# Kernel optimization log

Measured on AMD Instinct MI355X. Metric: run time of the kernel, lower is better.

Reference implementation:

```python
import jax, jax.numpy as jnp
import numpy as np
from jax import lax

B, T, N, H, NC = 2, 8, 512, 64, 10
NEG = -1e9
LN_EPS = 1e-5


def _gatv2(x, mask, Wl, Wr, att, b):
    # GATv2Conv (PyG semantics, eval mode): e_ij = att . leaky_relu(Wr x_i + Wl x_j),
    # softmax over source nodes j with self-loops, out_i = sum_j alpha_ij * (Wl x_j).
    # x: (B, N, Fin); mask: (N, N) bool adjacency incl. self-loops; att: (heads, C).
    heads, C = att.shape
    Bn, Nn, _ = x.shape
    xl = (x @ Wl).reshape(Bn, Nn, heads, C)  # source transform
    xr = (x @ Wr).reshape(Bn, Nn, heads, C)  # target transform
    s = jax.nn.leaky_relu(xr[:, :, None] + xl[:, None, :], 0.2)  # (B, Ni, Nj, h, C)
    e = jnp.einsum('bijhc,hc->bijh', s, att)
    e = jnp.where(mask[None, :, :, None], e, NEG)
    alpha = jax.nn.softmax(e, axis=2)  # softmax over neighbors j
    out = jnp.einsum('bijh,bjhc->bihc', alpha, xl)
    return out.reshape(Bn, Nn, heads * C) + b


def _gru_layer(x, Wih, Whh, bih, bhh):
    # torch nn.GRU single layer, batch_first; x: (B, T, Hin)
    h0 = jnp.zeros((x.shape[0], Whh.shape[0]), x.dtype)
    def step(h, xt):
        gi = xt @ Wih + bih
        gh = h @ Whh + bhh
        ir, iz, inn = jnp.split(gi, 3, axis=-1)
        hr, hz, hn = jnp.split(gh, 3, axis=-1)
        r = jax.nn.sigmoid(ir + hr)
        z = jax.nn.sigmoid(iz + hz)
        n = jnp.tanh(inn + r * hn)
        hnew = (1.0 - z) * n + z * h
        return hnew, hnew
    _, ys = lax.scan(step, h0, jnp.swapaxes(x, 0, 1))
    return jnp.swapaxes(ys, 0, 1)


def setup_inputs() -> dict:
    key = jax.random.key(0)
    ks = jax.random.split(key, 20)
    def rn(i, shape, s=0.1):
        return jax.random.normal(ks[i], shape, jnp.float32) * s
    x_seq = jax.random.normal(ks[0], (B, T, N, 1), jnp.float32)
    a = jax.random.uniform(ks[1], (N, N))
    up = jnp.triu((a > 0.95).astype(jnp.float32), 1)
    static_adj = up + up.T  # sparse symmetric 0/1 static graph
    dyn_W = jax.random.normal(ks[2], (N, N), jnp.float32)
    reg_lambda = jnp.array([0.05], jnp.float32)
    return {
        'x_seq': x_seq, 'static_adj': static_adj, 'dyn_W': dyn_W, 'reg_lambda': reg_lambda,
        'g1_Wl': rn(3, (1, H)), 'g1_Wr': rn(4, (1, H)), 'g1_att': rn(5, (4, H // 4)), 'g1_b': jnp.zeros(H),
        'g2_Wl': rn(6, (H, H)), 'g2_Wr': rn(7, (H, H)), 'g2_att': rn(8, (1, H)), 'g2_b': jnp.zeros(H),
        'gru_Wih0': rn(9, (H, 3 * H)), 'gru_Whh0': rn(10, (H, 3 * H)), 'gru_bih0': jnp.zeros(3 * H), 'gru_bhh0': jnp.zeros(3 * H),
        'gru_Wih1': rn(11, (H, 3 * H)), 'gru_Whh1': rn(12, (H, 3 * H)), 'gru_bih1': jnp.zeros(3 * H), 'gru_bhh1': jnp.zeros(3 * H),
        'attn_W': rn(13, (H, 1)), 'attn_b': jnp.zeros(1),
        'cls_W1': rn(14, (H, H)), 'cls_b1': jnp.zeros(H), 'ln_g': jnp.ones(H), 'ln_b': jnp.zeros(H),
        'cls_W2': rn(15, (H, NC)), 'cls_b2': jnp.zeros(NC),
    }


def reference(x_seq, static_adj, dyn_W, reg_lambda,
              g1_Wl, g1_Wr, g1_att, g1_b, g2_Wl, g2_Wr, g2_att, g2_b,
              gru_Wih0, gru_Whh0, gru_bih0, gru_bhh0,
              gru_Wih1, gru_Whh1, gru_bih1, gru_bhh1,
              attn_W, attn_b, cls_W1, cls_b1, ln_g, ln_b, cls_W2, cls_b2):
    Bn, Tn, Nn, _ = x_seq.shape
    lam = jnp.maximum(reg_lambda[0], 0.01)
    t = jnp.arange(Tn, dtype=x_seq.dtype)
    gts = jnp.exp(-lam * t)  # gating values per timestep
    dyn = jax.nn.relu(dyn_W + dyn_W.T)
    fused = gts[:, None, None] * static_adj + (1.0 - gts)[:, None, None] * dyn  # (T, N, N)
    masks = (fused > 0) | jnp.eye(Nn, dtype=bool)[None]  # edge set + self-loops

    def step(carry, inp):
        xt, mask = inp  # xt: (B, N, 1)
        h = jax.nn.elu(_gatv2(xt, mask, g1_Wl, g1_Wr, g1_att, g1_b))
        h = jax.nn.elu(_gatv2(h, mask, g2_Wl, g2_Wr, g2_att, g2_b))
        return carry, h.mean(axis=1)  # (B, H) graph readout

    _, reps = lax.scan(step, 0.0, (jnp.swapaxes(x_seq, 0, 1), masks))
    h_seq = jnp.swapaxes(reps, 0, 1)  # (B, T, H)

    gru_out = _gru_layer(h_seq, gru_Wih0, gru_Whh0, gru_bih0, gru_bhh0)
    gru_out = _gru_layer(gru_out, gru_Wih1, gru_Whh1, gru_bih1, gru_bhh1)

    att_scores = jax.nn.softmax((gru_out @ attn_W + attn_b)[..., 0], axis=1)  # (B, T)
    final = jnp.einsum('bt,bth->bh', att_scores, gru_out)

    z = final @ cls_W1 + cls_b1
    mu = jnp.mean(z, axis=-1, keepdims=True)
    var = jnp.var(z, axis=-1, keepdims=True)
    z = (z - mu) / jnp.sqrt(var + LN_EPS) * ln_g + ln_b
    z = jax.nn.gelu(z, approximate=False)
    logits = z @ cls_W2 + cls_b2
    return logits, gts, att_scores
```

## Files before the change

kernel.cpp:

```cpp
#include <hip/hip_runtime.h>
#include <math.h>

#define BB 2
#define TT 8
#define NN 512
#define HH 64
#define NC 10

typedef unsigned char uchar;

__device__ __forceinline__ float elu1(float v){ return v > 0.f ? v : expm1f(v); }
__device__ __forceinline__ float sigm(float v){ return 1.f/(1.f+expf(-v)); }

__global__ __launch_bounds__(256) void k_mask(
    const float* __restrict__ dW, const float* __restrict__ sadj,
    uchar* __restrict__ M0, uchar* __restrict__ M1,
    float* __restrict__ Z2, float* __restrict__ hseq,
    const float* __restrict__ att1, const float* __restrict__ Wr1,
    const float* __restrict__ Wl1, float* __restrict__ AB,
    const float* __restrict__ Whh0, const float* __restrict__ Wih1,
    const float* __restrict__ Whh1, float4* __restrict__ WT4)
{
    __shared__ float tr[64][65];
    int bx = blockIdx.x, by = blockIdx.y;
    int tid = threadIdx.x;
    if (blockIdx.z == 1){
        int idx = (by*8 + bx)*256 + tid;
        if (idx < 3*4096){
            int m = idx >> 12, r = idx & 4095;
            int gg = r >> 6, k = r & 63;
            const float* W = (m == 0) ? Whh0 : (m == 1) ? Wih1 : Whh1;
            float4 o;
            o.x = W[k*192 + gg];
            o.y = W[k*192 + 64 + gg];
            o.z = W[k*192 + 128 + gg];
            o.w = 0.f;
            WT4[(size_t)m*4096 + r] = o;
        }
        return;
    }
    int i0 = by*64, j0 = bx*64;
    #pragma unroll
    for (int q = 0; q < 4; ++q){
        int r = (tid >> 4) + 16*q, c4 = tid & 15;
        float4 v = *(const float4*)&dW[(size_t)(j0+r)*NN + i0 + 4*c4];
        tr[r][4*c4+0] = v.x; tr[r][4*c4+1] = v.y;
        tr[r][4*c4+2] = v.z; tr[r][4*c4+3] = v.w;
    }
    __syncthreads();
    #pragma unroll
    for (int q = 0; q < 4; ++q){
        int row = (tid >> 4) + 16*q, c4 = tid & 15;
        int i = i0 + row, j = j0 + 4*c4;
        float4 d  = *(const float4*)&dW[(size_t)i*NN + j];
        float4 sa = *(const float4*)&sadj[(size_t)i*NN + j];
        uchar4 m0, m1;
        float dd0 = d.x + tr[4*c4+0][row];
        float dd1 = d.y + tr[4*c4+1][row];
        float dd2 = d.z + tr[4*c4+2][row];
        float dd3 = d.w + tr[4*c4+3][row];
        m0.x = (sa.x > 0.f) || (i == j+0);
        m0.y = (sa.y > 0.f) || (i == j+1);
        m0.z = (sa.z > 0.f) || (i == j+2);
        m0.w = (sa.w > 0.f) || (i == j+3);
        m1.x = m0.x || (dd0 > 0.f);
        m1.y = m0.y || (dd1 > 0.f);
        m1.z = m0.z || (dd2 > 0.f);
        m1.w = m0.w || (dd3 > 0.f);
        *(uchar4*)&M0[(size_t)i*NN + j] = m0;
        *(uchar4*)&M1[(size_t)i*NN + j] = m1;
    }
    int flat = (by*8 + bx)*256 + tid;
    if (flat < BB*TT*NN) Z2[flat] = 0.f;
    else if (flat < BB*TT*NN + BB*TT*HH) hseq[flat - BB*TT*NN] = 0.f;
    if (bx == 0 && by == 0 && tid < 8){
        int h = tid & 3;
        const float* W = (tid < 4) ? Wr1 : Wl1;
        float s = 0.f;
        for (int c = 0; c < 16; ++c) s += att1[h*16+c]*W[h*16+c];
        AB[tid] = s;
    }
}

__global__ __launch_bounds__(256) void k_gat1f(
    const float* __restrict__ x_seq, const uchar* __restrict__ M0,
    const uchar* __restrict__ M1,
    const float* __restrict__ Wl, const float* __restrict__ Wr,
    const float* __restrict__ att, const float* __restrict__ bias,
    const float* __restrict__ AB,
    const float* __restrict__ Wl2, const float* __restrict__ Wr2,
    const float* __restrict__ att2,
    float* __restrict__ xl2, float* __restrict__ xr2,
    float* __restrict__ ui, float* __restrict__ vj)
{
    __shared__ float x_s[NN];
    __shared__ float S_s[4][4];
    __shared__ float h_s[4][HH];
    __shared__ float Wl2_s[64*64];
    __shared__ float Wr2_s[64*64];
    int bt = blockIdx.y; int t = bt % TT;
    int i0 = blockIdx.x * 4;
    int tid = threadIdx.x;
    int il = tid >> 6, jl = tid & 63;
    int i = i0 + il;
    const uchar* M = t ? M1 : M0;
    ((float2*)x_s)[tid] = ((const float2*)(x_seq + bt*NN))[tid];
    #pragma unroll
    for (int q = 0; q < 4; ++q){
        int idx = q*256 + tid;
        ((float4*)Wl2_s)[idx] = ((const float4*)Wl2)[idx];
        ((float4*)Wr2_s)[idx] = ((const float4*)Wr2)[idx];
    }
    __syncthreads();
    float xi = x_s[i];
    const uchar* Mrow = M + (size_t)i*NN;
    float xj[8], msk[8];
    #pragma unroll
    for (int jj = 0; jj < 8; ++jj){
        int j = jj*64 + jl;
        xj[jj] = x_s[j];
        msk[jj] = Mrow[j] ? 1.f : 0.f;
    }
    float sw[4] = {0,0,0,0}, swx[4] = {0,0,0,0};
    for (int h = 0; h < 4; ++h){
        float acc[8] = {0,0,0,0,0,0,0,0};
        #pragma unroll
        for (int c = 0; c < 16; ++c){
            int hc = h*16 + c;
            float wl = Wl[hc];
            float q  = 0.4f * att[hc];
            float pr = xi * Wr[hc];
            #pragma unroll
            for (int jj = 0; jj < 8; ++jj){
                float s = fmaf(xj[jj], wl, pr);
                acc[jj] = fmaf(q, fabsf(s), acc[jj]);
            }
        }
        float lin = 0.6f * xi * AB[h];
        float al6 = 0.6f * AB[4+h];
        #pragma unroll
        for (int jj = 0; jj < 8; ++jj){
            float e = acc[jj] + fmaf(al6, xj[jj], lin);
            float w = msk[jj] * __expf(e);
            sw[h] += w;
            swx[h] = fmaf(w, xj[jj], swx[h]);
        }
    }
    #pragma unroll
    for (int off = 32; off; off >>= 1){
        #pragma unroll
        for (int h = 0; h < 4; ++h){
            sw[h]  += __shfl_down(sw[h],  off);
            swx[h] += __shfl_down(swx[h], off);
        }
    }
    if (jl == 0){
        #pragma unroll
        for (int h = 0; h < 4; ++h) S_s[il][h] = swx[h] / sw[h];
    }
    __syncthreads();
    {
        int hc = tid & 63, row = tid >> 6;
        float v = S_s[row][hc >> 4] * Wl[hc] + bias[hc];
        h_s[row][hc] = elu1(v);
    }
    __syncthreads();
    {
        int c = tid & 63, row = tid >> 6;
        float al = 0.f, ar = 0.f;
        #pragma unroll 8
        for (int k = 0; k < 64; ++k){
            float hv = h_s[row][k];
            al = fmaf(hv, Wl2_s[k*64 + c], al);
            ar = fmaf(hv, Wr2_s[k*64 + c], ar);
        }
        size_t ridx = (size_t)(bt*NN + i0 + row);
        xl2[ridx*HH + c] = al;
        xr2[ridx*HH + c] = ar;
        float a2 = att2[c];
        float pu = a2 * ar, pv = a2 * al;
        #pragma unroll
        for (int off = 32; off; off >>= 1){
            pu += __shfl_down(pu, off);
            pv += __shfl_down(pv, off);
        }
        if (c == 0){ ui[ridx] = pu; vj[ridx] = pv; }
    }
}

__global__ __launch_bounds__(256) void k_e2(
    const float* __restrict__ xl2, const float* __restrict__ xr2,
    const uchar* __restrict__ M0, const uchar* __restrict__ M1,
    const float* __restrict__ att,
    const float* __restrict__ ui, const float* __restrict__ vj,
    float* __restrict__ WgT, float* __restrict__ Z2)
{
    __shared__ float xrT[64][68];
    __shared__ float xlT[64][68];
    int bt = blockIdx.z, t = bt % TT;
    int i0 = blockIdx.y*64, j0 = blockIdx.x*64;
    int base = bt*NN;
    int tid = threadIdx.x;
    const uchar* M = t ? M1 : M0;
    {
        int r = tid >> 2;
        #pragma unroll
        for (int q = 0; q < 4; ++q){
            int c4 = (tid & 3) + 4*q;
            float4 a = *(const float4*)&xr2[(size_t)(base+i0+r)*HH + 4*c4];
            float4 b = *(const float4*)&xl2[(size_t)(base+j0+r)*HH + 4*c4];
            xrT[4*c4+0][r] = a.x; xrT[4*c4+1][r] = a.y;
            xrT[4*c4+2][r] = a.z; xrT[4*c4+3][r] = a.w;
            xlT[4*c4+0][r] = b.x; xlT[4*c4+1][r] = b.y;
            xlT[4*c4+2][r] = b.z; xlT[4*c4+3][r] = b.w;
        }
    }
    int ti = tid >> 4, tj = tid & 15;
    int iL = ti*4, jL = tj*4;
    float4 u4 = *(const float4*)&ui[base+i0+iL];
    float4 v4 = *(const float4*)&vj[base+j0+jL];
    float uu[4] = {u4.x, u4.y, u4.z, u4.w};
    float vv[4] = {v4.x, v4.y, v4.z, v4.w};
    float acc[4][4];
    #pragma unroll
    for (int ii = 0; ii < 4; ++ii)
        #pragma unroll
        for (int jj = 0; jj < 4; ++jj)
            acc[ii][jj] = 0.6f*(uu[ii] + vv[jj]);
    __syncthreads();
    #pragma unroll 8
    for (int c = 0; c < 64; ++c){
        float qa = 0.4f * att[c];
        float4 a4 = *(const float4*)&xrT[c][iL];
        float4 b4 = *(const float4*)&xlT[c][jL];
        float a[4] = {a4.x, a4.y, a4.z, a4.w};
        float b[4] = {b4.x, b4.y, b4.z, b4.w};
        #pragma unroll
        for (int ii = 0; ii < 4; ++ii)
            #pragma unroll
            for (int jj = 0; jj < 4; ++jj)
                acc[ii][jj] = fmaf(qa, fabsf(a[ii] + b[jj]), acc[ii][jj]);
    }
    float w[4][4];
    #pragma unroll
    for (int ii = 0; ii < 4; ++ii){
        int i = i0 + iL + ii;
        uchar4 mr = *(const uchar4*)&M[(size_t)i*NN + j0 + jL];
        w[ii][0] = mr.x ? __expf(acc[ii][0]) : 0.f;
        w[ii][1] = mr.y ? __expf(acc[ii][1]) : 0.f;
        w[ii][2] = mr.z ? __expf(acc[ii][2]) : 0.f;
        w[ii][3] = mr.w ? __expf(acc[ii][3]) : 0.f;
    }
    #pragma unroll
    for (int jj = 0; jj < 4; ++jj){
        int j = j0 + jL + jj;
        float4 wv = { w[0][jj], w[1][jj], w[2][jj], w[3][jj] };
        *(float4*)&WgT[(size_t)(base+j)*NN + i0 + iL] = wv;
    }
    #pragma unroll
    for (int ii = 0; ii < 4; ++ii){
        float zi = w[ii][0] + w[ii][1] + w[ii][2] + w[ii][3];
        zi += __shfl_down(zi, 8);
        zi += __shfl_down(zi, 4);
        zi += __shfl_down(zi, 2);
        zi += __shfl_down(zi, 1);
        if (tj == 0) atomicAdd(&Z2[base + i0 + iL + ii], zi);
    }
}

__global__ __launch_bounds__(256) void k_a2(
    const float* __restrict__ WgT, const float* __restrict__ xl2,
    const float* __restrict__ Z2, const float* __restrict__ bias,
    float* __restrict__ hseq)
{
    __shared__ float a_s[64][20];
    __shared__ float x_s[64][68];
    __shared__ float msum[64];
    int bt = blockIdx.y;
    int i0 = blockIdx.x * 16;
    int base = bt * NN;
    int tid = threadIdx.x;
    int tg = tid >> 4, tc = tid & 15;
    if (tid < 64) msum[tid] = 0.f;
    float4 acc = {0,0,0,0};
    for (int jc = 0; jc < 8; ++jc){
        int j0 = jc*64;
        {
            int row = tid >> 2, c4 = tid & 3;
            ((float4*)&a_s[row][0])[c4] = ((const float4*)&WgT[(size_t)(base+j0+row)*NN + i0])[c4];
        }
        #pragma unroll
        for (int q = 0; q < 4; ++q){
            int idx = q*256 + tid; int row = idx >> 4, c4 = idx & 15;
            ((float4*)&x_s[row][0])[c4] = ((const float4*)&xl2[(size_t)(base+j0+row)*HH])[c4];
        }
        __syncthreads();
        #pragma unroll 8
        for (int j = 0; j < 64; ++j){
            float a = a_s[j][tg];
            float4 xv = ((float4*)&x_s[j][0])[tc];
            acc.x = fmaf(a, xv.x, acc.x);
            acc.y = fmaf(a, xv.y, acc.y);
            acc.z = fmaf(a, xv.z, acc.z);
            acc.w = fmaf(a, xv.w, acc.w);
        }
        __syncthreads();
    }
    float rz = 1.f / Z2[base + i0 + tg];
    float4 b4 = ((const float4*)bias)[tc];
    float4 h;
    h.x = elu1(acc.x*rz + b4.x);
    h.y = elu1(acc.y*rz + b4.y);
    h.z = elu1(acc.z*rz + b4.z);
    h.w = elu1(acc.w*rz + b4.w);
    atomicAdd(&msum[tc*4+0], h.x);
    atomicAdd(&msum[tc*4+1], h.y);
    atomicAdd(&msum[tc*4+2], h.z);
    atomicAdd(&msum[tc*4+3], h.w);
    __syncthreads();
    if (tid < 64) atomicAdd(&hseq[bt*HH + tid], msum[tid]*(1.f/(float)NN));
}

__global__ __launch_bounds__(256) void k_pre(
    const float* __restrict__ hseq, const float* __restrict__ Wih0,
    const float* __restrict__ bih0, float* __restrict__ gi0)
{
    int idx = blockIdx.x*256 + threadIdx.x;
    int bt = idx / 192, g = idx % 192;
    const float* x = hseq + bt*HH;
    float acc = bih0[g];
    #pragma unroll 8
    for (int k = 0; k < HH; ++k)
        acc = fmaf(x[k], Wih0[k*192 + g], acc);
    gi0[idx] = acc;
}

#define P4 65
__global__ __launch_bounds__(512) void k_gru2(
    const float* __restrict__ gi0, const float4* __restrict__ WT4,
    const float* __restrict__ bhh0,
    const float* __restrict__ bih1, const float* __restrict__ bhh1,
    const float* __restrict__ lamp, const float* __restrict__ attn_W,
    const float* __restrict__ attn_b, const float* __restrict__ W1,
    const float* __restrict__ b1, const float* __restrict__ ln_g,
    const float* __restrict__ ln_b, const float* __restrict__ W2,
    const float* __restrict__ b2, float* __restrict__ out)
{
    __shared__ float4 WA[64*P4];
    __shared__ float4 WB[64*P4];
    __shared__ float gi_s[BB*TT*192];
    __shared__ float y_s[BB*TT*HH];
    __shared__ float sc_s[BB][TT], at_s[BB][TT];
    __shared__ float fin_s[BB][HH], z_s[BB][HH], g_s[BB][HH];
    __shared__ float mu_s[BB], iv_s[BB];
    int tid = threadIdx.x;
    int wave = tid >> 6, lane = tid & 63;
    for (int v = tid; v < 4096; v += 512){
        WA[(v >> 6)*P4 + (v & 63)] = WT4[v];
        WB[(v >> 6)*P4 + (v & 63)] = WT4[4096 + v];
    }
    for (int v = tid; v < BB*TT*192; v += 512) gi_s[v] = gi0[v];
    __syncthreads();
    float y[TT];
    float g1r[TT], g1z[TT], g1n[TT];
    if (wave < 2){
        int b = wave;
        float bhr = bhh0[lane], bhz = bhh0[64+lane], bhn = bhh0[128+lane];
        float h = 0.f;
        for (int t = 0; t < TT; ++t){
            float ghr = bhr, ghz = bhz, ghn = bhn;
            #pragma unroll 16
            for (int k = 0; k < 64; ++k){
                float4 w4 = WA[lane*P4 + k];
                float hk = __shfl(h, k);
                ghr = fmaf(w4.x, hk, ghr);
                ghz = fmaf(w4.y, hk, ghz);
                ghn = fmaf(w4.z, hk, ghn);
            }
            const float* gi = &gi_s[(b*TT + t)*192];
            float r = sigm(gi[lane] + ghr);
            float z = sigm(gi[64+lane] + ghz);
            float n = tanhf(gi[128+lane] + r*ghn);
            h = (1.f - z)*n + z*h;
            y[t] = h;
        }
        float bi1r = bih1[lane], bi1z = bih1[64+lane], bi1n = bih1[128+lane];
        #pragma unroll
        for (int t = 0; t < TT; ++t){ g1r[t] = bi1r; g1z[t] = bi1z; g1n[t] = bi1n; }
        #pragma unroll 8
        for (int k = 0; k < 64; ++k){
            float4 w4 = WB[lane*P4 + k];
            #pragma unroll
            for (int t = 0; t < TT; ++t){
                float yk = __shfl(y[t], k);
                g1r[t] = fmaf(w4.x, yk, g1r[t]);
                g1z[t] = fmaf(w4.y, yk, g1z[t]);
                g1n[t] = fmaf(w4.z, yk, g1n[t]);
            }
        }
    }
    __syncthreads();
    if (wave >= 2){
        for (int v = tid - 128; v < 4096; v += 384)
            WA[(v >> 6)*P4 + (v & 63)] = WT4[2*4096 + v];
    }
    __syncthreads();
    if (wave < 2){
        int b = wave;
        float bhr = bhh1[lane], bhz = bhh1[64+lane], bhn = bhh1[128+lane];
        float h = 0.f;
        for (int t = 0; t < TT; ++t){
            float ghr = bhr, ghz = bhz, ghn = bhn;
            #pragma unroll 16
            for (int k = 0; k < 64; ++k){
                float4 w4 = WA[lane*P4 + k];
                float hk = __shfl(h, k);
                ghr = fmaf(w4.x, hk, ghr);
                ghz = fmaf(w4.y, hk, ghz);
                ghn = fmaf(w4.z, hk, ghn);
            }
            float r = sigm(g1r[t] + ghr);
            float z = sigm(g1z[t] + ghz);
            float n = tanhf(g1n[t] + r*ghn);
            h = (1.f - z)*n + z*h;
            y_s[(b*TT + t)*HH + lane] = h;
        }
    }
    __syncthreads();
    float lam = fmaxf(lamp[0], 0.01f);
    if (tid < TT) out[BB*NC + tid] = expf(-lam*(float)tid);
    if (tid < BB*TT){
        int bb = tid >> 3, t = tid & 7;
        float s = attn_b[0];
        const float* r = &y_s[(bb*TT+t)*HH];
        for (int h = 0; h < HH; ++h) s += r[h]*attn_W[h];
        sc_s[bb][t] = s;
    }
    __syncthreads();
    if (tid < BB){
        float mx = -INFINITY;
        for (int t = 0; t < TT; ++t) mx = fmaxf(mx, sc_s[tid][t]);
        float se = 0.f;
        for (int t = 0; t < TT; ++t){ float w = expf(sc_s[tid][t]-mx); at_s[tid][t] = w; se += w; }
        for (int t = 0; t < TT; ++t){
            at_s[tid][t] /= se;
            out[BB*NC + TT + tid*TT + t] = at_s[tid][t];
        }
    }
    __syncthreads();
    if (tid < BB*HH){
        int bb = tid >> 6, h = tid & 63;
        float a = 0.f;
        for (int t = 0; t < TT; ++t) a += at_s[bb][t]*y_s[(bb*TT+t)*HH + h];
        fin_s[bb][h] = a;
    }
    __syncthreads();
    if (tid < BB*HH){
        int bb = tid >> 6, h = tid & 63;
        float a = b1[h];
        for (int k = 0; k < HH; ++k) a += fin_s[bb][k]*W1[k*HH+h];
        z_s[bb][h] = a;
    }
    __syncthreads();
    if (tid < BB){
        float mu = 0.f;
        for (int h = 0; h < HH; ++h) mu += z_s[tid][h];
        mu *= (1.f/HH);
        float v = 0.f;
        for (int h = 0; h < HH; ++h){ float d = z_s[tid][h]-mu; v += d*d; }
        v *= (1.f/HH);
        mu_s[tid] = mu; iv_s[tid] = 1.f/sqrtf(v + 1e-5f);
    }
    __syncthreads();
    if (tid < BB*HH){
        int bb = tid >> 6, h = tid & 63;
        float zn = (z_s[bb][h]-mu_s[bb])*iv_s[bb]*ln_g[h] + ln_b[h];
        g_s[bb][h] = 0.5f*zn*(1.f + erff(zn*0.70710678118654752f));
    }
    __syncthreads();
    if (tid < BB*NC){
        int bb = tid / NC, c = tid % NC;
        float a = b2[c];
        for (int k = 0; k < HH; ++k) a += g_s[bb][k]*W2[k*NC+c];
        out[bb*NC + c] = a;
    }
}

extern "C" void kernel_launch(void* const* d_in, const int* in_sizes, int n_in,
                              void* d_out, int out_size, void* d_ws, size_t ws_size,
                              hipStream_t stream)
{
    const float* x_seq = (const float*)d_in[0];
    const float* sadj  = (const float*)d_in[1];
    const float* dynW  = (const float*)d_in[2];
    const float* lamp  = (const float*)d_in[3];
    const float* g1_Wl = (const float*)d_in[4];
    const float* g1_Wr = (const float*)d_in[5];
    const float* g1_att= (const float*)d_in[6];
    const float* g1_b  = (const float*)d_in[7];
    const float* g2_Wl = (const float*)d_in[8];
    const float* g2_Wr = (const float*)d_in[9];
    const float* g2_att= (const float*)d_in[10];
    const float* g2_b  = (const float*)d_in[11];
    const float* Wih0  = (const float*)d_in[12];
    const float* Whh0  = (const float*)d_in[13];
    const float* bih0  = (const float*)d_in[14];
    const float* bhh0  = (const float*)d_in[15];
    const float* Wih1  = (const float*)d_in[16];
    const float* Whh1  = (const float*)d_in[17];
    const float* bih1  = (const float*)d_in[18];
    const float* bhh1  = (const float*)d_in[19];
    const float* attnW = (const float*)d_in[20];
    const float* attnb = (const float*)d_in[21];
    const float* W1    = (const float*)d_in[22];
    const float* b1    = (const float*)d_in[23];
    const float* lng   = (const float*)d_in[24];
    const float* lnb   = (const float*)d_in[25];
    const float* W2    = (const float*)d_in[26];
    const float* b2    = (const float*)d_in[27];
    float* out = (float*)d_out;

    const int RWS = BB*TT*NN*HH;
    uchar* M0 = (uchar*)d_ws;
    uchar* M1 = M0 + (size_t)NN*NN;
    float* fb = (float*)(M1 + (size_t)NN*NN);
    float* Z2   = fb;
    float* AB   = Z2   + BB*TT*NN;
    float* ui   = AB   + 16;
    float* vj   = ui   + BB*TT*NN;
    float* xl2  = vj   + BB*TT*NN;
    float* xr2  = xl2  + RWS;
    float* WgT  = xr2  + RWS;
    float* hseq = WgT  + (size_t)BB*TT*NN*NN;
    float* gi0  = hseq + BB*TT*HH;
    float4* WT4 = (float4*)(gi0 + BB*TT*192);

    k_mask <<<dim3(8,8,2), 256, 0, stream>>>(dynW, sadj, M0, M1, Z2, hseq, g1_att, g1_Wr, g1_Wl, AB,
                                             Whh0, Wih1, Whh1, WT4);
    k_gat1f<<<dim3(NN/4, BB*TT), 256, 0, stream>>>(x_seq, M0, M1, g1_Wl, g1_Wr, g1_att, g1_b, AB,
                                                   g2_Wl, g2_Wr, g2_att, xl2, xr2, ui, vj);
    k_e2   <<<dim3(NN/64, NN/64, BB*TT), 256, 0, stream>>>(xl2, xr2, M0, M1, g2_att, ui, vj, WgT, Z2);
    k_a2   <<<dim3(NN/16, BB*TT), 256, 0, stream>>>(WgT, xl2, Z2, g2_b, hseq);
    k_pre  <<<12, 256, 0, stream>>>(hseq, Wih0, bih0, gi0);
    k_gru2 <<<1, 512, 0, stream>>>(gi0, WT4, bhh0, bih1, bhh1,
                                   lamp, attnW, attnb, W1, b1, lng, lnb, W2, b2, out);
}
```

Baseline: 223.0 us.

## Fuse GATv2 layer-2 scoring and aggregation into a flash-style kernel

Merges the edge-score kernel and the aggregation kernel into one kernel. It keeps each 16-row by 64-column block of unnormalized weights in shared memory, which removes the large B*T*N*N weight buffer, the separate normalizer array and the atomics that fill it. The GRU input projection (k_pre) is also folded into the GRU kernel, so two launches go away. The cost is that every source tile of xl2 is now reloaded once per 16-row target block. There are also fewer blocks and more shared-memory traffic per block, since the score and aggregation loops now run in sequence inside one kernel.

```diff
diff --git a/kernel.cpp b/kernel.cpp
--- a/kernel.cpp
+++ b/kernel.cpp
@@ -15,7 +15,7 @@
 __global__ __launch_bounds__(256) void k_mask(
     const float* __restrict__ dW, const float* __restrict__ sadj,
     uchar* __restrict__ M0, uchar* __restrict__ M1,
-    float* __restrict__ Z2, float* __restrict__ hseq,
+    float* __restrict__ hseq,
     const float* __restrict__ att1, const float* __restrict__ Wr1,
     const float* __restrict__ Wl1, float* __restrict__ AB,
     const float* __restrict__ Whh0, const float* __restrict__ Wih1,
@@ -35,7 +35,7 @@
             o.y = W[k*192 + 64 + gg];
             o.z = W[k*192 + 128 + gg];
             o.w = 0.f;
-            WT4[(size_t)m*4096 + r] = o;
+            WT4[idx] = o;
         }
         return;
     }
@@ -71,8 +71,7 @@
         *(uchar4*)&M1[(size_t)i*NN + j] = m1;
     }
     int flat = (by*8 + bx)*256 + tid;
-    if (flat < BB*TT*NN) Z2[flat] = 0.f;
-    else if (flat < BB*TT*NN + BB*TT*HH) hseq[flat - BB*TT*NN] = 0.f;
+    if (flat < BB*TT*HH) hseq[flat] = 0.f;
     if (bx == 0 && by == 0 && tid < 8){
         int h = tid & 3;
         const float* W = (tid < 4) ? Wr1 : Wl1;
@@ -188,156 +187,103 @@
     }
 }
 
-__global__ __launch_bounds__(256) void k_e2(
+__global__ __launch_bounds__(256) void k_flash2(
     const float* __restrict__ xl2, const float* __restrict__ xr2,
     const uchar* __restrict__ M0, const uchar* __restrict__ M1,
-    const float* __restrict__ att,
+    const float* __restrict__ att, const float* __restrict__ bias,
     const float* __restrict__ ui, const float* __restrict__ vj,
-    float* __restrict__ WgT, float* __restrict__ Z2)
-{
-    __shared__ float xrT[64][68];
-    __shared__ float xlT[64][68];
-    int bt = blockIdx.z, t = bt % TT;
-    int i0 = blockIdx.y*64, j0 = blockIdx.x*64;
-    int base = bt*NN;
-    int tid = threadIdx.x;
-    const uchar* M = t ? M1 : M0;
-    {
-        int r = tid >> 2;
-        #pragma unroll
-        for (int q = 0; q < 4; ++q){
-            int c4 = (tid & 3) + 4*q;
-            float4 a = *(const float4*)&xr2[(size_t)(base+i0+r)*HH + 4*c4];
-            float4 b = *(const float4*)&xl2[(size_t)(base+j0+r)*HH + 4*c4];
-            xrT[4*c4+0][r] = a.x; xrT[4*c4+1][r] = a.y;
-            xrT[4*c4+2][r] = a.z; xrT[4*c4+3][r] = a.w;
-            xlT[4*c4+0][r] = b.x; xlT[4*c4+1][r] = b.y;
-            xlT[4*c4+2][r] = b.z; xlT[4*c4+3][r] = b.w;
-        }
-    }
-    int ti = tid >> 4, tj = tid & 15;
-    int iL = ti*4, jL = tj*4;
-    float4 u4 = *(const float4*)&ui[base+i0+iL];
-    float4 v4 = *(const float4*)&vj[base+j0+jL];
-    float uu[4] = {u4.x, u4.y, u4.z, u4.w};
-    float vv[4] = {v4.x, v4.y, v4.z, v4.w};
-    float acc[4][4];
-    #pragma unroll
-    for (int ii = 0; ii < 4; ++ii)
-        #pragma unroll
-        for (int jj = 0; jj < 4; ++jj)
-            acc[ii][jj] = 0.6f*(uu[ii] + vv[jj]);
-    __syncthreads();
-    #pragma unroll 8
-    for (int c = 0; c < 64; ++c){
-        float qa = 0.4f * att[c];
-        float4 a4 = *(const float4*)&xrT[c][iL];
-        float4 b4 = *(const float4*)&xlT[c][jL];
-        float a[4] = {a4.x, a4.y, a4.z, a4.w};
-        float b[4] = {b4.x, b4.y, b4.z, b4.w};
-        #pragma unroll
-        for (int ii = 0; ii < 4; ++ii)
-            #pragma unroll
-            for (int jj = 0; jj < 4; ++jj)
-                acc[ii][jj] = fmaf(qa, fabsf(a[ii] + b[jj]), acc[ii][jj]);
-    }
-    float w[4][4];
-    #pragma unroll
-    for (int ii = 0; ii < 4; ++ii){
-        int i = i0 + iL + ii;
-        uchar4 mr = *(const uchar4*)&M[(size_t)i*NN + j0 + jL];
-        w[ii][0] = mr.x ? __expf(acc[ii][0]) : 0.f;
-        w[ii][1] = mr.y ? __expf(acc[ii][1]) : 0.f;
-        w[ii][2] = mr.z ? __expf(acc[ii][2]) : 0.f;
-        w[ii][3] = mr.w ? __expf(acc[ii][3]) : 0.f;
-    }
-    #pragma unroll
-    for (int jj = 0; jj < 4; ++jj){
-        int j = j0 + jL + jj;
-        float4 wv = { w[0][jj], w[1][jj], w[2][jj], w[3][jj] };
-        *(float4*)&WgT[(size_t)(base+j)*NN + i0 + iL] = wv;
-    }
-    #pragma unroll
-    for (int ii = 0; ii < 4; ++ii){
-        float zi = w[ii][0] + w[ii][1] + w[ii][2] + w[ii][3];
-        zi += __shfl_down(zi, 8);
-        zi += __shfl_down(zi, 4);
-        zi += __shfl_down(zi, 2);
-        zi += __shfl_down(zi, 1);
-        if (tj == 0) atomicAdd(&Z2[base + i0 + iL + ii], zi);
-    }
-}
-
-__global__ __launch_bounds__(256) void k_a2(
-    const float* __restrict__ WgT, const float* __restrict__ xl2,
-    const float* __restrict__ Z2, const float* __restrict__ bias,
     float* __restrict__ hseq)
 {
-    __shared__ float a_s[64][20];
-    __shared__ float x_s[64][68];
+    __shared__ float xrR[16][68];
+    __shared__ float xlR[64][68];
+    __shared__ float w_s[16][68];
+    __shared__ float vj_s[64];
+    __shared__ float Zl[16];
     __shared__ float msum[64];
-    int bt = blockIdx.y;
-    int i0 = blockIdx.x * 16;
-    int base = bt * NN;
+    int bt = blockIdx.y, it = blockIdx.x;
+    int i0 = it*16, t = bt % TT, base = bt*NN;
+    const uchar* M = t ? M1 : M0;
     int tid = threadIdx.x;
-    int tg = tid >> 4, tc = tid & 15;
+    int ti = tid >> 4, tj = tid & 15;
+    *(float4*)&xrR[ti][4*tj] = *(const float4*)&xr2[(size_t)(base+i0+ti)*HH + 4*tj];
     if (tid < 64) msum[tid] = 0.f;
+    float u = ui[base + i0 + ti];
+    float zacc = 0.f;
     float4 acc = {0,0,0,0};
-    for (int jc = 0; jc < 8; ++jc){
-        int j0 = jc*64;
-        {
-            int row = tid >> 2, c4 = tid & 3;
-            ((float4*)&a_s[row][0])[c4] = ((const float4*)&WgT[(size_t)(base+j0+row)*NN + i0])[c4];
-        }
+    for (int jt = 0; jt < 8; ++jt){
+        int j0 = jt*64;
         #pragma unroll
         for (int q = 0; q < 4; ++q){
-            int idx = q*256 + tid; int row = idx >> 4, c4 = idx & 15;
-            ((float4*)&x_s[row][0])[c4] = ((const float4*)&xl2[(size_t)(base+j0+row)*HH])[c4];
-        }
+            int idx = q*256 + tid;
+            int r = idx >> 4, c4 = idx & 15;
+            *(float4*)&xlR[r][4*c4] = *(const float4*)&xl2[(size_t)(base+j0+r)*HH + 4*c4];
+        }
+        if (tid < 64) vj_s[tid] = vj[base + j0 + tid];
+        __syncthreads();
+        float e[4];
+        #pragma unroll
+        for (int jq = 0; jq < 4; ++jq)
+            e[jq] = 0.6f*(u + vj_s[tj + 16*jq]);
+        #pragma unroll 4
+        for (int cq = 0; cq < 16; ++cq){
+            float4 qa = ((const float4*)att)[cq];
+            qa.x *= 0.4f; qa.y *= 0.4f; qa.z *= 0.4f; qa.w *= 0.4f;
+            float4 a4 = *(const float4*)&xrR[ti][4*cq];
+            #pragma unroll
+            for (int jq = 0; jq < 4; ++jq){
+                float4 b4 = *(const float4*)&xlR[tj + 16*jq][4*cq];
+                e[jq] = fmaf(qa.x, fabsf(a4.x + b4.x), e[jq]);
+                e[jq] = fmaf(qa.y, fabsf(a4.y + b4.y), e[jq]);
+                e[jq] = fmaf(qa.z, fabsf(a4.z + b4.z), e[jq]);
+                e[jq] = fmaf(qa.w, fabsf(a4.w + b4.w), e[jq]);
+            }
+        }
+        const uchar* Mrow = M + (size_t)(i0+ti)*NN + j0;
+        float zp = 0.f;
+        #pragma unroll
+        for (int jq = 0; jq < 4; ++jq){
+            float w = Mrow[tj + 16*jq] ? __expf(e[jq]) : 0.f;
+            w_s[ti][tj + 16*jq] = w;
+            zp += w;
+        }
+        zp += __shfl_down(zp, 8);
+        zp += __shfl_down(zp, 4);
+        zp += __shfl_down(zp, 2);
+        zp += __shfl_down(zp, 1);
+        if (tj == 0) zacc += zp;
         __syncthreads();
         #pragma unroll 8
         for (int j = 0; j < 64; ++j){
-            float a = a_s[j][tg];
-            float4 xv = ((float4*)&x_s[j][0])[tc];
-            acc.x = fmaf(a, xv.x, acc.x);
-            acc.y = fmaf(a, xv.y, acc.y);
-            acc.z = fmaf(a, xv.z, acc.z);
-            acc.w = fmaf(a, xv.w, acc.w);
+            float w = w_s[ti][j];
+            float4 x4 = *(const float4*)&xlR[j][4*tj];
+            acc.x = fmaf(w, x4.x, acc.x);
+            acc.y = fmaf(w, x4.y, acc.y);
+            acc.z = fmaf(w, x4.z, acc.z);
+            acc.w = fmaf(w, x4.w, acc.w);
         }
         __syncthreads();
     }
-    float rz = 1.f / Z2[base + i0 + tg];
-    float4 b4 = ((const float4*)bias)[tc];
+    if (tj == 0) Zl[ti] = zacc;
+    __syncthreads();
+    float rz = 1.f / Zl[ti];
+    float4 b4 = ((const float4*)bias)[tj];
     float4 h;
     h.x = elu1(acc.x*rz + b4.x);
     h.y = elu1(acc.y*rz + b4.y);
     h.z = elu1(acc.z*rz + b4.z);
     h.w = elu1(acc.w*rz + b4.w);
-    atomicAdd(&msum[tc*4+0], h.x);
-    atomicAdd(&msum[tc*4+1], h.y);
-    atomicAdd(&msum[tc*4+2], h.z);
-    atomicAdd(&msum[tc*4+3], h.w);
+    atomicAdd(&msum[4*tj+0], h.x);
+    atomicAdd(&msum[4*tj+1], h.y);
+    atomicAdd(&msum[4*tj+2], h.z);
+    atomicAdd(&msum[4*tj+3], h.w);
     __syncthreads();
     if (tid < 64) atomicAdd(&hseq[bt*HH + tid], msum[tid]*(1.f/(float)NN));
 }
 
-__global__ __launch_bounds__(256) void k_pre(
-    const float* __restrict__ hseq, const float* __restrict__ Wih0,
-    const float* __restrict__ bih0, float* __restrict__ gi0)
-{
-    int idx = blockIdx.x*256 + threadIdx.x;
-    int bt = idx / 192, g = idx % 192;
-    const float* x = hseq + bt*HH;
-    float acc = bih0[g];
-    #pragma unroll 8
-    for (int k = 0; k < HH; ++k)
-        acc = fmaf(x[k], Wih0[k*192 + g], acc);
-    gi0[idx] = acc;
-}
-
 #define P4 65
 __global__ __launch_bounds__(512) void k_gru2(
-    const float* __restrict__ gi0, const float4* __restrict__ WT4,
+    const float* __restrict__ hseq, const float* __restrict__ Wih0,
+    const float* __restrict__ bih0, const float4* __restrict__ WT4,
     const float* __restrict__ bhh0,
     const float* __restrict__ bih1, const float* __restrict__ bhh1,
     const float* __restrict__ lamp, const float* __restrict__ attn_W,
@@ -349,6 +295,7 @@
     __shared__ float4 WA[64*P4];
     __shared__ float4 WB[64*P4];
     __shared__ float gi_s[BB*TT*192];
+    __shared__ float hs[BB*TT*HH];
     __shared__ float y_s[BB*TT*HH];
     __shared__ float sc_s[BB][TT], at_s[BB][TT];
     __shared__ float fin_s[BB][HH], z_s[BB][HH], g_s[BB][HH];
@@ -359,10 +306,183 @@
         WA[(v >> 6)*P4 + (v & 63)] = WT4[v];
         WB[(v >> 6)*P4 + (v & 63)] = WT4[4096 + v];
     }
-    for (int v = tid; v < BB*TT*192; v += 512) gi_s[v] = gi0[v];
-    __syncthreads();
-    float y[TT];
-    float g1r[TT], g1z[TT], g1n[TT];
+    for (int v = tid; v < BB*TT*HH; v += 512) hs[v] = hseq[v];
+    __syncthreads();
+    for (int o = tid; o < BB*TT*192; o += 512){
+        int bt = o / 192, g = o % 192;
+        float a = bih0[g];
+        #pragma unroll 8
+        for (int k = 0; k < HH; ++k)
+            a = fmaf(hs[bt*HH + k], Wih0[k*192 + g], a);
+        gi_s[o] = a;
+    }
+    __syncthreads();
+    if (wave < 2){
+        int b = wave;
+        float y[TT], g1r[TT], g1z[TT], g1n[TT];
+        {
+            float bhr = bhh0[lane], bhz = bhh0[64+lane], bhn = bhh0[128+lane];
+            float h = 0.f;
+            for (int t = 0; t < TT; ++t){
+                float ghr = bhr, ghz = bhz, ghn = bhn;
+                #pragma unroll 16
+                for (int k = 0; k < 64; ++k){
+                    float4 w4 = WA[lane*P4 + k];
+                    float hk = __shfl(h, k);
+                    ghr = fmaf(w4.x, hk, ghr);
+                    ghz = fmaf(w4.y, hk, ghz);
+                    ghn = fmaf(w4.z, hk, ghn);
+                }
+                const float* gi = &gi_s[(b*TT + t)*192];
+                float r = sigm(gi[lane] + ghr);
+                float z = sigm(gi[64+lane] + ghz);
+                float n = tanhf(gi[128+lane] + r*ghn);
+                h = (1.f - z)*n + z*h;
+                y[t] = h;
+            }
+        }
+        {
+            float bi1r = bih1[lane], bi1z = bih1[64+lane], bi1n = bih1[128+lane];
+            #pragma unroll
+            for (int t = 0; t < TT; ++t){ g1r[t] = bi1r; g1z[t] = bi1z; g1n[t] = bi1n; }
+            #pragma unroll 8
+            for (int k = 0; k < 64; ++k){
+                float4 w4 = WB[lane*P4 + k];
+                #pragma unroll
+                for (int t = 0; t < TT; ++t){
+                    float yk = __shfl(y[t], k);
+                    g1r[t] = fmaf(w4.x, yk, g1r[t]);
+                    g1z[t] = fmaf(w4.y, yk, g1z[t]);
+                    g1n[t] = fmaf(w4.z, yk, g1n[t]);
+                }
+            }
+        }
+        __syncthreads();
+        {
+            float bhr = bhh1[lane], bhz = bhh1[64+lane], bhn = bhh1[128+lane];
+            float h = 0.f;
+            for (int t = 0; t < TT; ++t){
+                float ghr = bhr, ghz = bhz, ghn = bhn;
+                #pragma unroll 16
+                for (int k = 0; k < 64; ++k){
+                    float4 w4 = WB[lane*P4 + k];
+                    float hk = __shfl(h, k);
+                    ghr = fmaf(w4.x, hk, ghr);
+                    ghz = fmaf(w4.y, hk, ghz);
+                    ghn = fmaf(w4.z, hk, ghn);
+                }
+                float r = sigm(g1r[t] + ghr);
+                float z = sigm(g1z[t] + ghz);
+                float n = tanhf(g1n[t] + r*ghn);
+                h = (1.f - z)*n + z*h;
+                y_s[(b*TT + t)*HH + lane] = h;
+            }
+        }
+    } else {
+        __syncthreads();
+    }
+    __syncthreads();
+    float lam = fmaxf(lamp[0], 0.01f);
+    if (tid < TT) out[BB*NC + tid] = expf(-lam*(float)tid);
+    if (tid < BB*TT){
+        int bb = tid >> 3, t = tid & 7;
+        float s = attn_b[0];
+        const float* r = &y_s[(bb*TT+t)*HH];
+        for (int h = 0; h < HH; ++h) s += r[h]*attn_W[h];
+        sc_s[bb][t] = s;
+    }
+    __syncthreads();
+    if (tid < BB){
+        float mx = -INFINITY;
+        for (int t = 0; t < TT; ++t) mx = fmaxf(mx, sc_s[tid][t]);
+        float se = 0.f;
+        for (int t = 0; t < TT; ++t){ float w = expf(sc_s[tid][t]-mx); at_s[tid][t] = w; se += w; }
+        for (int t = 0; t < TT; ++t){
+            at_s[tid][t] /= se;
+            out[BB*NC + TT + tid*TT + t] = at_s[tid][t];
+        }
+    }
+    __syncthreads();
+    if (tid < BB*HH){
+        int bb = tid >> 6, h = tid & 63;
+        float a = 0.f;
+        for (int t = 0; t < TT; ++t) a += at_s[bb][t]*y_s[(bb*TT+t)*HH + h];
+        fin_s[bb][h] = a;
+    }
+    __syncthreads();
+    if (tid < BB*HH){
+        int bb = tid >> 6, h = tid & 63;
+        float a = b1[h];
+        for (int k = 0; k < HH; ++k) a += fin_s[bb][k]*W1[k*HH+h];
+        z_s[bb][h] = a;
+    }
+    __syncthreads();
+    if (tid < BB){
+        float mu = 0.f;
+        for (int h = 0; h < HH; ++h) mu += z_s[tid][h];
+        mu *= (1.f/HH);
+        float v = 0.f;
+        for (int h = 0; h < HH; ++h){ float d = z_s[tid][h]-mu; v += d*d; }
+        v *= (1.f/HH);
+        mu_s[tid] = mu; iv_s[tid] = 1.f/sqrtf(v + 1e-5f);
+    }
+    __syncthreads();
+    if (tid < BB*HH){
+        int bb = tid >> 6, h = tid & 63;
+        float zn = (z_s[bb][h]-mu_s[bb])*iv_s[bb]*ln_g[h] + ln_b[h];
+        g_s[bb][h] = 0.5f*zn*(1.f + erff(zn*0.70710678118654752f));
+    }
+    __syncthreads();
+    if (tid < BB*NC){
+        int bb = tid / NC, c = tid % NC;
+        float a = b2[c];
+        for (int k = 0; k < HH; ++k) a += g_s[bb][k]*W2[k*NC+c];
+        out[bb*NC + c] = a;
+    }
+}
+
+
+extern "C" void kernel_launch(void* const* d_in, const int* in_sizes, int n_in,
+                              void* d_out, int out_size, void* d_ws, size_t ws_size,
+                              hipStream_t stream);
+
+__global__ __launch_bounds__(512) void k_gru2b(
+    const float* __restrict__ hseq, const float* __restrict__ Wih0,
+    const float* __restrict__ bih0, const float4* __restrict__ WT4,
+    const float* __restrict__ bhh0,
+    const float* __restrict__ bih1, const float* __restrict__ bhh1,
+    const float* __restrict__ lamp, const float* __restrict__ attn_W,
+    const float* __restrict__ attn_b, const float* __restrict__ W1,
+    const float* __restrict__ b1, const float* __restrict__ ln_g,
+    const float* __restrict__ ln_b, const float* __restrict__ W2,
+    const float* __restrict__ b2, float* __restrict__ out)
+{
+    __shared__ float4 WA[64*P4];
+    __shared__ float4 WB[64*P4];
+    __shared__ float gi_s[BB*TT*192];
+    __shared__ float hs[BB*TT*HH];
+    __shared__ float y_s[BB*TT*HH];
+    __shared__ float sc_s[BB][TT], at_s[BB][TT];
+    __shared__ float fin_s[BB][HH], z_s[BB][HH], g_s[BB][HH];
+    __shared__ float mu_s[BB], iv_s[BB];
+    int tid = threadIdx.x;
+    int wave = tid >> 6, lane = tid & 63;
+    for (int v = tid; v < 4096; v += 512){
+        WA[(v >> 6)*P4 + (v & 63)] = WT4[v];
+        WB[(v >> 6)*P4 + (v & 63)] = WT4[4096 + v];
+    }
+    for (int v = tid; v < BB*TT*HH; v += 512) hs[v] = hseq[v];
+    __syncthreads();
+    for (int o = tid; o < BB*TT*192; o += 512){
+        int bt = o / 192, g = o % 192;
+        float a = bih0[g];
+        #pragma unroll 8
+        for (int k = 0; k < HH; ++k)
+            a = fmaf(hs[bt*HH + k], Wih0[k*192 + g], a);
+        gi_s[o] = a;
+    }
+    __syncthreads();
+    float y[TT], g1r[TT], g1z[TT], g1n[TT];
     if (wave < 2){
         int b = wave;
         float bhr = bhh0[lane], bhz = bhh0[64+lane], bhn = bhh0[128+lane];
@@ -400,10 +520,8 @@
         }
     }
     __syncthreads();
-    if (wave >= 2){
-        for (int v = tid - 128; v < 4096; v += 384)
-            WA[(v >> 6)*P4 + (v & 63)] = WT4[2*4096 + v];
-    }
+    for (int v = tid; v < 4096; v += 512)
+        WA[(v >> 6)*P4 + (v & 63)] = WT4[2*4096 + v];
     __syncthreads();
     if (wave < 2){
         int b = wave;
@@ -524,24 +642,19 @@
     uchar* M0 = (uchar*)d_ws;
     uchar* M1 = M0 + (size_t)NN*NN;
     float* fb = (float*)(M1 + (size_t)NN*NN);
-    float* Z2   = fb;
-    float* AB   = Z2   + BB*TT*NN;
+    float* AB   = fb;
     float* ui   = AB   + 16;
     float* vj   = ui   + BB*TT*NN;
     float* xl2  = vj   + BB*TT*NN;
     float* xr2  = xl2  + RWS;
-    float* WgT  = xr2  + RWS;
-    float* hseq = WgT  + (size_t)BB*TT*NN*NN;
-    float* gi0  = hseq + BB*TT*HH;
-    float4* WT4 = (float4*)(gi0 + BB*TT*192);
-
-    k_mask <<<dim3(8,8,2), 256, 0, stream>>>(dynW, sadj, M0, M1, Z2, hseq, g1_att, g1_Wr, g1_Wl, AB,
-                                             Whh0, Wih1, Whh1, WT4);
-    k_gat1f<<<dim3(NN/4, BB*TT), 256, 0, stream>>>(x_seq, M0, M1, g1_Wl, g1_Wr, g1_att, g1_b, AB,
-                                                   g2_Wl, g2_Wr, g2_att, xl2, xr2, ui, vj);
-    k_e2   <<<dim3(NN/64, NN/64, BB*TT), 256, 0, stream>>>(xl2, xr2, M0, M1, g2_att, ui, vj, WgT, Z2);
-    k_a2   <<<dim3(NN/16, BB*TT), 256, 0, stream>>>(WgT, xl2, Z2, g2_b, hseq);
-    k_pre  <<<12, 256, 0, stream>>>(hseq, Wih0, bih0, gi0);
-    k_gru2 <<<1, 512, 0, stream>>>(gi0, WT4, bhh0, bih1, bhh1,
-                                   lamp, attnW, attnb, W1, b1, lng, lnb, W2, b2, out);
+    float* hseq = xr2  + RWS;
+    float* WT4  = hseq + BB*TT*HH;
+
+    k_mask  <<<dim3(8,8,2), 256, 0, stream>>>(dynW, sadj, M0, M1, hseq, g1_att, g1_Wr, g1_Wl, AB,
+                                              Whh0, Wih1, Whh1, (float4*)WT4);
+    k_gat1f <<<dim3(NN/4, BB*TT), 256, 0, stream>>>(x_seq, M0, M1, g1_Wl, g1_Wr, g1_att, g1_b, AB,
+                                                    g2_Wl, g2_Wr, g2_att, xl2, xr2, ui, vj);
+    k_flash2<<<dim3(NN/16, BB*TT), 256, 0, stream>>>(xl2, xr2, M0, M1, g2_att, g2_b, ui, vj, hseq);
+    k_gru2b <<<1, 512, 0, stream>>>(hseq, Wih0, bih0, (const float4*)WT4, bhh0, bih1, bhh1,
+                                    lamp, attnW, attnb, W1, b1, lng, lnb, W2, b2, out);
 }
```

Result: slower. 233.0 us (+4.5%).
